# Optimization experiments

Measured on AMD Instinct MI355X. Metric: run time of the kernel, lower is better.

## Reference

```python
import jax, jax.numpy as jnp
import numpy as np

GRID = 100  # voxel index range per axis (coors drawn in [0, GRID))
N_POINTS = 1_000_000
N_FEAT = 64
MAX_VOXELS = N_POINTS  # static upper bound on number of unique voxels


def setup_inputs() -> dict:
    key = jax.random.key(0)
    kf, kc = jax.random.split(key)
    feats = jax.random.normal(kf, (N_POINTS, N_FEAT), dtype=jnp.float32)
    coors = jax.random.randint(kc, (N_POINTS, 3), 0, GRID, dtype=jnp.int32)
    return {"feats": feats, "coors": coors}


def reference(feats, coors):
    """Dynamic point-to-voxel scatter with 'mean' reduce (average_points=True).

    Returns (voxel_feats [M_max, C], voxel_coors [M_max, 3]).
    Unique-voxel rows are packed first (sorted by linear key); padded rows
    (beyond the true voxel count M) have zero features and coors == -1.
    """
    n = feats.shape[0]
    # linear hash of 3D voxel coordinate
    keys = (coors[:, 0].astype(jnp.int64) * GRID * GRID
            + coors[:, 1].astype(jnp.int64) * GRID
            + coors[:, 2].astype(jnp.int64))
    uniq, inv = jnp.unique(keys, size=MAX_VOXELS, fill_value=-1,
                           return_inverse=True)
    inv = inv.reshape(n)
    # per-voxel sum and count -> mean
    sums = jax.ops.segment_sum(feats, inv, num_segments=MAX_VOXELS)
    counts = jax.ops.segment_sum(jnp.ones((n,), dtype=feats.dtype), inv,
                                 num_segments=MAX_VOXELS)
    voxel_feats = sums / jnp.maximum(counts, 1.0)[:, None]
    # decode unique linear keys back to 3D voxel coordinates (-1 for padding)
    valid = uniq >= 0
    u = jnp.where(valid, uniq, 0)
    cx = (u // (GRID * GRID)).astype(jnp.int32)
    cy = ((u // GRID) % GRID).astype(jnp.int32)
    cz = (u % GRID).astype(jnp.int32)
    voxel_coors = jnp.stack([cx, cy, cz], axis=-1)
    voxel_coors = jnp.where(valid[:, None], voxel_coors, -1)
    voxel_feats = jnp.where(valid[:, None], voxel_feats, 0.0)
    return voxel_feats, voxel_coors
```

## Files before the change

### kernel.cpp

```cpp
#include <hip/hip_runtime.h>

#define NPTS   1000000
#define NFEAT  64
#define GRIDN  100
#define NBINS  1000000

#define SCAN_B    256
#define SCAN_I    4
#define SCAN_TILE 1024
#define NBLK      977

__global__ void k_count(const int* __restrict__ coors, int* __restrict__ keys,
                        int* __restrict__ count, int n) {
    int p = blockIdx.x * blockDim.x + threadIdx.x;
    if (p >= n) return;
    int c0 = coors[p * 3 + 0];
    int c1 = coors[p * 3 + 1];
    int c2 = coors[p * 3 + 2];
    int key = (c0 * GRIDN + c1) * GRIDN + c2;
    keys[p] = key;
    atomicAdd(&count[key], 1);
}

__global__ void k_scan1(const int4* __restrict__ count4, int* __restrict__ blkOcc,
                        int* __restrict__ blkCnt) {
    __shared__ int sO[SCAN_B], sC[SCAN_B];
    int tid  = threadIdx.x;
    int base = blockIdx.x * SCAN_TILE + tid * SCAN_I;
    int tO = 0, tC = 0;
    if (base < NBINS) {
        int4 v = count4[base >> 2];
        tO = (v.x > 0) + (v.y > 0) + (v.z > 0) + (v.w > 0);
        tC = v.x + v.y + v.z + v.w;
    }
    sO[tid] = tO; sC[tid] = tC;
    __syncthreads();
    for (int ofs = SCAN_B / 2; ofs > 0; ofs >>= 1) {
        if (tid < ofs) { sO[tid] += sO[tid + ofs]; sC[tid] += sC[tid + ofs]; }
        __syncthreads();
    }
    if (tid == 0) { blkOcc[blockIdx.x] = sO[0]; blkCnt[blockIdx.x] = sC[0]; }
}

__global__ void k_scan2(int* __restrict__ blkOcc, int* __restrict__ blkCnt,
                        int* __restrict__ m_dev) {
    __shared__ int sO[1024], sC[1024];
    int tid = threadIdx.x;
    int vO = (tid < NBLK) ? blkOcc[tid] : 0;
    int vC = (tid < NBLK) ? blkCnt[tid] : 0;
    sO[tid] = vO; sC[tid] = vC;
    __syncthreads();
    for (int ofs = 1; ofs < 1024; ofs <<= 1) {
        int a = 0, b = 0;
        if (tid >= ofs) { a = sO[tid - ofs]; b = sC[tid - ofs]; }
        __syncthreads();
        sO[tid] += a; sC[tid] += b;
        __syncthreads();
    }
    if (tid < NBLK) {
        blkOcc[tid] = sO[tid] - vO;
        blkCnt[tid] = sC[tid] - vC;
    }
    if (tid == 1023) *m_dev = sO[1023];
}

__global__ void k_scan3(const int4* __restrict__ count4, int4* __restrict__ pstart4,
                        const int* __restrict__ blkOcc, const int* __restrict__ blkCnt,
                        long long* __restrict__ rankstart, int4* __restrict__ rowinfo) {
    __shared__ int sO[SCAN_B], sC[SCAN_B];
    int tid  = threadIdx.x;
    int base = blockIdx.x * SCAN_TILE + tid * SCAN_I;
    int4 v = make_int4(0, 0, 0, 0);
    if (base < NBINS) v = count4[base >> 2];
    int c[SCAN_I] = {v.x, v.y, v.z, v.w};
    int locO[SCAN_I], locC[SCAN_I];
    int tO = 0, tC = 0;
    #pragma unroll
    for (int i = 0; i < SCAN_I; ++i) {
        locO[i] = tO; locC[i] = tC;
        tO += (c[i] > 0) ? 1 : 0;
        tC += c[i];
    }
    sO[tid] = tO; sC[tid] = tC;
    __syncthreads();
    for (int ofs = 1; ofs < SCAN_B; ofs <<= 1) {
        int a = 0, b = 0;
        if (tid >= ofs) { a = sO[tid - ofs]; b = sC[tid - ofs]; }
        __syncthreads();
        sO[tid] += a; sC[tid] += b;
        __syncthreads();
    }
    if (base >= NBINS) return;
    int exO = sO[tid] - tO + blkOcc[blockIdx.x];
    int exC = sC[tid] - tC + blkCnt[blockIdx.x];
    int4 ps;
    ps.x = exC + locC[0]; ps.y = exC + locC[1];
    ps.z = exC + locC[2]; ps.w = exC + locC[3];
    pstart4[base >> 2] = ps;
    int psa[SCAN_I] = {ps.x, ps.y, ps.z, ps.w};
    #pragma unroll
    for (int i = 0; i < SCAN_I; ++i) {
        if (c[i] > 0) {
            int bin = base + i;
            int r   = exO + locO[i];
            rankstart[bin] = ((long long)r << 32) | (long long)psa[i];
            *(int2*)(&rowinfo[r]) = make_int2(psa[i], bin | (c[i] << 20));
        }
    }
}

__global__ void k_fill(const int* __restrict__ keys, int* __restrict__ pstart,
                       const long long* __restrict__ rankstart,
                       int* __restrict__ perm, int4* __restrict__ rowinfo, int n) {
    int p = blockIdx.x * blockDim.x + threadIdx.x;
    if (p >= n) return;
    int k = keys[p];
    int pos = atomicAdd(&pstart[k], 1);
    long long rs = rankstart[k];
    int start = (int)(rs & 0xFFFFFFFFLL);
    int r     = (int)(rs >> 32);
    int j = pos - start;
    if (j < 2) ((int*)rowinfo)[r * 4 + 2 + j] = p;
    else       perm[pos] = p;
}

__global__ void k_mean(const float4* __restrict__ feats4,
                       const int4* __restrict__ rowinfo,
                       const int* __restrict__ perm,
                       const int* __restrict__ m_dev,
                       float4* __restrict__ out4) {
    int gid = blockIdx.x * blockDim.x + threadIdx.x;
    int row = gid >> 4;
    int sub = gid & 15;
    if (row >= NBINS) return;
    float* out_coors = (float*)(out4 + (size_t)NBINS * 16);
    int M = *m_dev;
    if (row < M) {
        int4 info = rowinfo[row];
        int start = info.x;
        int bin   = info.y & 0xFFFFF;
        int cnt   = info.y >> 20;
        float4 s = feats4[(size_t)info.z * 16 + sub];
        if (cnt > 1) {
            float4 f = feats4[(size_t)info.w * 16 + sub];
            s.x += f.x; s.y += f.y; s.z += f.z; s.w += f.w;
        }
        if (cnt > 2) {
            int gbase = (threadIdx.x & 63) & ~15;
            for (int b0 = 2; b0 < cnt; b0 += 16) {
                int rem = cnt - b0;
                int lim = rem < 16 ? rem : 16;
                int pv  = (sub < lim) ? perm[start + b0 + sub] : 0;
                for (int j = 0; j < lim; ++j) {
                    int pj = __shfl(pv, gbase + j);
                    float4 f = feats4[(size_t)pj * 16 + sub];
                    s.x += f.x; s.y += f.y; s.z += f.z; s.w += f.w;
                }
            }
        }
        float inv = 1.0f / (float)cnt;
        s.x *= inv; s.y *= inv; s.z *= inv; s.w *= inv;
        out4[(size_t)row * 16 + sub] = s;
        if (sub < 3) {
            int v = (sub == 0) ? bin / (GRIDN * GRIDN)
                  : (sub == 1) ? (bin / GRIDN) % GRIDN
                  :               bin % GRIDN;
            out_coors[row * 3 + sub] = (float)v;
        }
    } else {
        out4[(size_t)row * 16 + sub] = make_float4(0.f, 0.f, 0.f, 0.f);
        if (sub < 3) out_coors[row * 3 + sub] = -1.f;
    }
}

extern "C" void kernel_launch(void* const* d_in, const int* in_sizes, int n_in,
                              void* d_out, int out_size, void* d_ws, size_t ws_size,
                              hipStream_t stream) {
    const float* feats = (const float*)d_in[0];
    const int*   coors = (const int*)d_in[1];
    float*       out   = (float*)d_out;
    int n = in_sizes[1] / 3;

    int*       keys      = (int*)d_ws;
    int*       count     = keys   + NPTS;
    int*       pstart    = count  + NBINS;
    int*       perm      = pstart + NBINS;
    int4*      rowinfo   = (int4*)(perm + NPTS);
    long long* rankstart = (long long*)(rowinfo + NBINS);
    int*       blkOcc    = (int*)(rankstart + NBINS);
    int*       blkCnt    = blkOcc + NBLK;
    int*       m_dev     = blkCnt + NBLK;

    hipMemsetAsync(count, 0, NBINS * sizeof(int), stream);

    int b = 256;
    k_count<<<(n + b - 1) / b, b, 0, stream>>>(coors, keys, count, n);
    k_scan1<<<NBLK, SCAN_B, 0, stream>>>((const int4*)count, blkOcc, blkCnt);
    k_scan2<<<1, 1024, 0, stream>>>(blkOcc, blkCnt, m_dev);
    k_scan3<<<NBLK, SCAN_B, 0, stream>>>((const int4*)count, (int4*)pstart,
                                         blkOcc, blkCnt, rankstart, rowinfo);
    k_fill<<<(n + b - 1) / b, b, 0, stream>>>(keys, pstart, rankstart, perm,
                                              rowinfo, n);
    k_mean<<<(NBINS * 16) / b, b, 0, stream>>>((const float4*)feats, rowinfo, perm,
                                               m_dev, (float4*)out);
}
```

Measured before the change: 557.0 us.

## Vectorize count/fill over four points, skip atomics for singleton voxels, nontemporal feature I/O

k_count and k_fill now have each thread handle four points, with int4 loads of coordinates and keys. rankstart also packs the bin count, so k_fill writes a singleton voxel's point index straight into rowinfo without the atomicAdd on pstart. k_mean switches to ext_vector float types with nontemporal loads and stores for features and output, and launch bounds are added to all kernels. The four-wide split assumes n is divisible by four, and the packing limits start offsets to 20 bits and counts to 12 bits.

```diff
diff --git a/kernel.cpp b/kernel.cpp
--- a/kernel.cpp
+++ b/kernel.cpp
@@ -10,20 +10,30 @@
 #define SCAN_TILE 1024
 #define NBLK      977
 
-__global__ void k_count(const int* __restrict__ coors, int* __restrict__ keys,
-                        int* __restrict__ count, int n) {
-    int p = blockIdx.x * blockDim.x + threadIdx.x;
-    if (p >= n) return;
-    int c0 = coors[p * 3 + 0];
-    int c1 = coors[p * 3 + 1];
-    int c2 = coors[p * 3 + 2];
-    int key = (c0 * GRIDN + c1) * GRIDN + c2;
-    keys[p] = key;
-    atomicAdd(&count[key], 1);
-}
-
-__global__ void k_scan1(const int4* __restrict__ count4, int* __restrict__ blkOcc,
-                        int* __restrict__ blkCnt) {
+typedef float f4 __attribute__((ext_vector_type(4)));
+
+__global__ __launch_bounds__(256) void k_count(const int4* __restrict__ coors4,
+                                               int4* __restrict__ keys4,
+                                               int* __restrict__ count, int nq) {
+    int t = blockIdx.x * blockDim.x + threadIdx.x;
+    if (t >= nq) return;
+    int4 a = coors4[3 * t + 0];
+    int4 b = coors4[3 * t + 1];
+    int4 c = coors4[3 * t + 2];
+    int k0 = (a.x * GRIDN + a.y) * GRIDN + a.z;
+    int k1 = (a.w * GRIDN + b.x) * GRIDN + b.y;
+    int k2 = (b.z * GRIDN + b.w) * GRIDN + c.x;
+    int k3 = (c.y * GRIDN + c.z) * GRIDN + c.w;
+    keys4[t] = make_int4(k0, k1, k2, k3);
+    atomicAdd(&count[k0], 1);
+    atomicAdd(&count[k1], 1);
+    atomicAdd(&count[k2], 1);
+    atomicAdd(&count[k3], 1);
+}
+
+__global__ __launch_bounds__(256) void k_scan1(const int4* __restrict__ count4,
+                                               int* __restrict__ blkOcc,
+                                               int* __restrict__ blkCnt) {
     __shared__ int sO[SCAN_B], sC[SCAN_B];
     int tid  = threadIdx.x;
     int base = blockIdx.x * SCAN_TILE + tid * SCAN_I;
@@ -42,8 +52,9 @@
     if (tid == 0) { blkOcc[blockIdx.x] = sO[0]; blkCnt[blockIdx.x] = sC[0]; }
 }
 
-__global__ void k_scan2(int* __restrict__ blkOcc, int* __restrict__ blkCnt,
-                        int* __restrict__ m_dev) {
+__global__ __launch_bounds__(1024) void k_scan2(int* __restrict__ blkOcc,
+                                                int* __restrict__ blkCnt,
+                                                int* __restrict__ m_dev) {
     __shared__ int sO[1024], sC[1024];
     int tid = threadIdx.x;
     int vO = (tid < NBLK) ? blkOcc[tid] : 0;
@@ -64,9 +75,12 @@
     if (tid == 1023) *m_dev = sO[1023];
 }
 
-__global__ void k_scan3(const int4* __restrict__ count4, int4* __restrict__ pstart4,
-                        const int* __restrict__ blkOcc, const int* __restrict__ blkCnt,
-                        long long* __restrict__ rankstart, int4* __restrict__ rowinfo) {
+__global__ __launch_bounds__(256) void k_scan3(const int4* __restrict__ count4,
+                                               int4* __restrict__ pstart4,
+                                               const int* __restrict__ blkOcc,
+                                               const int* __restrict__ blkCnt,
+                                               long long* __restrict__ rankstart,
+                                               int4* __restrict__ rowinfo) {
     __shared__ int sO[SCAN_B], sC[SCAN_B];
     int tid  = threadIdx.x;
     int base = blockIdx.x * SCAN_TILE + tid * SCAN_I;
@@ -103,32 +117,48 @@
         if (c[i] > 0) {
             int bin = base + i;
             int r   = exO + locO[i];
-            rankstart[bin] = ((long long)r << 32) | (long long)psa[i];
+            rankstart[bin] = ((long long)r << 32)
+                           | (long long)(unsigned)((c[i] << 20) | psa[i]);
             *(int2*)(&rowinfo[r]) = make_int2(psa[i], bin | (c[i] << 20));
         }
     }
 }
 
-__global__ void k_fill(const int* __restrict__ keys, int* __restrict__ pstart,
-                       const long long* __restrict__ rankstart,
-                       int* __restrict__ perm, int4* __restrict__ rowinfo, int n) {
-    int p = blockIdx.x * blockDim.x + threadIdx.x;
-    if (p >= n) return;
-    int k = keys[p];
-    int pos = atomicAdd(&pstart[k], 1);
-    long long rs = rankstart[k];
-    int start = (int)(rs & 0xFFFFFFFFLL);
-    int r     = (int)(rs >> 32);
-    int j = pos - start;
-    if (j < 2) ((int*)rowinfo)[r * 4 + 2 + j] = p;
-    else       perm[pos] = p;
-}
-
-__global__ void k_mean(const float4* __restrict__ feats4,
-                       const int4* __restrict__ rowinfo,
-                       const int* __restrict__ perm,
-                       const int* __restrict__ m_dev,
-                       float4* __restrict__ out4) {
+__global__ __launch_bounds__(256) void k_fill(const int4* __restrict__ keys4,
+                                              int* __restrict__ pstart,
+                                              const long long* __restrict__ rankstart,
+                                              int* __restrict__ perm,
+                                              int4* __restrict__ rowinfo, int nq) {
+    int t = blockIdx.x * blockDim.x + threadIdx.x;
+    if (t >= nq) return;
+    int4 kv = keys4[t];
+    int ks[4] = {kv.x, kv.y, kv.z, kv.w};
+    long long rs[4];
+    #pragma unroll
+    for (int i = 0; i < 4; ++i) rs[i] = rankstart[ks[i]];
+    int pbase = t * 4;
+    #pragma unroll
+    for (int i = 0; i < 4; ++i) {
+        int start = (int)(rs[i] & 0xFFFFF);
+        int cnt   = (int)((rs[i] >> 20) & 0xFFF);
+        int r     = (int)(rs[i] >> 32);
+        int p     = pbase + i;
+        if (cnt == 1) {
+            ((int*)rowinfo)[r * 4 + 2] = p;
+        } else {
+            int pos = atomicAdd(&pstart[ks[i]], 1);
+            int j = pos - start;
+            if (j < 2) ((int*)rowinfo)[r * 4 + 2 + j] = p;
+            else       perm[pos] = p;
+        }
+    }
+}
+
+__global__ __launch_bounds__(256) void k_mean(const f4* __restrict__ feats4,
+                                              const int4* __restrict__ rowinfo,
+                                              const int* __restrict__ perm,
+                                              const int* __restrict__ m_dev,
+                                              f4* __restrict__ out4) {
     int gid = blockIdx.x * blockDim.x + threadIdx.x;
     int row = gid >> 4;
     int sub = gid & 15;
@@ -140,10 +170,10 @@
         int start = info.x;
         int bin   = info.y & 0xFFFFF;
         int cnt   = info.y >> 20;
-        float4 s = feats4[(size_t)info.z * 16 + sub];
+        f4 s = __builtin_nontemporal_load(&feats4[(size_t)info.z * 16 + sub]);
         if (cnt > 1) {
-            float4 f = feats4[(size_t)info.w * 16 + sub];
-            s.x += f.x; s.y += f.y; s.z += f.z; s.w += f.w;
+            f4 f = __builtin_nontemporal_load(&feats4[(size_t)info.w * 16 + sub]);
+            s += f;
         }
         if (cnt > 2) {
             int gbase = (threadIdx.x & 63) & ~15;
@@ -153,14 +183,14 @@
                 int pv  = (sub < lim) ? perm[start + b0 + sub] : 0;
                 for (int j = 0; j < lim; ++j) {
                     int pj = __shfl(pv, gbase + j);
-                    float4 f = feats4[(size_t)pj * 16 + sub];
-                    s.x += f.x; s.y += f.y; s.z += f.z; s.w += f.w;
+                    f4 f = __builtin_nontemporal_load(&feats4[(size_t)pj * 16 + sub]);
+                    s += f;
                 }
             }
         }
         float inv = 1.0f / (float)cnt;
-        s.x *= inv; s.y *= inv; s.z *= inv; s.w *= inv;
-        out4[(size_t)row * 16 + sub] = s;
+        s *= inv;
+        __builtin_nontemporal_store(s, &out4[(size_t)row * 16 + sub]);
         if (sub < 3) {
             int v = (sub == 0) ? bin / (GRIDN * GRIDN)
                   : (sub == 1) ? (bin / GRIDN) % GRIDN
@@ -168,7 +198,8 @@
             out_coors[row * 3 + sub] = (float)v;
         }
     } else {
-        out4[(size_t)row * 16 + sub] = make_float4(0.f, 0.f, 0.f, 0.f);
+        f4 z = (f4){0.f, 0.f, 0.f, 0.f};
+        __builtin_nontemporal_store(z, &out4[(size_t)row * 16 + sub]);
         if (sub < 3) out_coors[row * 3 + sub] = -1.f;
     }
 }
@@ -193,14 +224,16 @@
 
     hipMemsetAsync(count, 0, NBINS * sizeof(int), stream);
 
-    int b = 256;
-    k_count<<<(n + b - 1) / b, b, 0, stream>>>(coors, keys, count, n);
+    int b  = 256;
+    int nq = n >> 2;
+    k_count<<<(nq + b - 1) / b, b, 0, stream>>>((const int4*)coors, (int4*)keys,
+                                                count, nq);
     k_scan1<<<NBLK, SCAN_B, 0, stream>>>((const int4*)count, blkOcc, blkCnt);
     k_scan2<<<1, 1024, 0, stream>>>(blkOcc, blkCnt, m_dev);
     k_scan3<<<NBLK, SCAN_B, 0, stream>>>((const int4*)count, (int4*)pstart,
                                          blkOcc, blkCnt, rankstart, rowinfo);
-    k_fill<<<(n + b - 1) / b, b, 0, stream>>>(keys, pstart, rankstart, perm,
-                                              rowinfo, n);
-    k_mean<<<(NBINS * 16) / b, b, 0, stream>>>((const float4*)feats, rowinfo, perm,
-                                               m_dev, (float4*)out);
-}
+    k_fill<<<(nq + b - 1) / b, b, 0, stream>>>((const int4*)keys, pstart, rankstart,
+                                               perm, rowinfo, nq);
+    k_mean<<<(NBINS * 16) / b, b, 0, stream>>>((const f4*)feats, rowinfo, perm,
+                                               m_dev, (f4*)out);
+}
```

Result: faster. 537.6 us (-3.5%).
